# Optimization experiments

Measured on AMD Instinct MI355X. Metric: run time of the kernel, lower is better.

## Reference

```python
import jax, jax.numpy as jnp
import numpy as np

N_NODES = 100000
N_EDGES = 3200000
D = 128
B = 4


def gcn_conv(x, row, col, W, b, n):
    # PyG GCNConv: x' = D^{-1/2}(A+I)D^{-1/2} (x W) + b
    xw = x @ W  # [N, out]
    ones = jnp.ones((row.shape[0],), dtype=x.dtype)
    deg = jax.ops.segment_sum(ones, col, num_segments=n) + 1.0  # self-loop
    dinv = jax.lax.rsqrt(deg)  # deg > 0 because of self-loops
    norm = dinv[row] * dinv[col]  # [E]
    msg = xw[row] * norm[:, None]  # gather + scale
    agg = jax.ops.segment_sum(msg, col, num_segments=n)  # scatter-add
    agg = agg + (dinv * dinv)[:, None] * xw  # self-loop contribution
    return agg + b


def setup_inputs() -> dict:
    key = jax.random.key(0)
    ks = jax.random.split(key, 10)
    x = jax.random.normal(ks[0], (N_NODES, D), dtype=jnp.float32)
    edge_index = jax.random.randint(ks[1], (2, N_EDGES), 0, N_NODES, dtype=jnp.int64)
    question_embeddings = jax.random.normal(ks[2], (B, D), dtype=jnp.float32)
    s = 1.0 / np.sqrt(D)
    W1 = jax.random.uniform(ks[3], (D, D), jnp.float32, -s, s)
    b1 = jnp.zeros((D,), jnp.float32)
    W2 = jax.random.uniform(ks[4], (D, D), jnp.float32, -s, s)
    b2 = jnp.zeros((D,), jnp.float32)
    Wq = jax.random.uniform(ks[5], (D, D), jnp.float32, -s, s)
    bq = jax.random.uniform(ks[6], (D,), jnp.float32, -s, s)
    return {"x": x, "edge_index": edge_index, "question_embeddings": question_embeddings,
            "W1": W1, "b1": b1, "W2": W2, "b2": b2, "Wq": Wq, "bq": bq}


def reference(x, edge_index, question_embeddings, W1, b1, W2, b2, Wq, bq):
    n = x.shape[0]
    row, col = edge_index[0], edge_index[1]
    h = jax.nn.relu(gcn_conv(x, row, col, W1, b1, n))  # [N, H]
    h = gcn_conv(h, row, col, W2, b2, n)  # [N, H]
    q = question_embeddings @ Wq + bq  # [B, H]
    out = h[None, :, :] + q[:, None, :]  # [B, N, H]
    return jax.nn.log_softmax(out, axis=1)  # softmax over node dim (torch dim=1)
```

## Files before the change

### kernel.cpp

```cpp
#include <hip/hip_runtime.h>
#include <math.h>

#define DD 128
#define CT 4096
#define CAP 10240

typedef unsigned int uint;
typedef unsigned short u16;

typedef __attribute__((ext_vector_type(8))) __bf16 bf16x8;
typedef __attribute__((ext_vector_type(2))) __bf16 bf16x2;
typedef __attribute__((ext_vector_type(4))) float f32x4;
typedef __attribute__((ext_vector_type(4))) uint uint4v;
typedef __attribute__((ext_vector_type(8))) u16 u16x8;


__device__ inline uint bf16bits(float a) {
  uint u = __float_as_uint(a);
  return (u + 0x7fffu + ((u >> 16) & 1u)) >> 16;
}

__device__ inline uint pack_bf16x2(float a, float b) {
  bf16x2 t;
  t[0] = (__bf16)a;
  t[1] = (__bf16)b;
  return __builtin_bit_cast(uint, t);
}

__device__ inline float lo16f(uint u) { return __uint_as_float(u << 16); }
__device__ inline float hi16f(uint u) { return __uint_as_float(u & 0xffff0000u); }


__global__ __launch_bounds__(256) void k_coarse(const int* __restrict__ row,
                                                const int* __restrict__ col,
                                                int* __restrict__ gcursor,
                                                uint* __restrict__ coarse,
                                                int E, int NB) {
  __shared__ int hist[512];
  __shared__ int base[512];
  int tid = threadIdx.x;
  long e0 = (long)blockIdx.x * CT;
  int cnt = (int)min((long)CT, (long)E - e0);
  int cnt4 = cnt >> 2;
  const int4* c4p = (const int4*)(col + e0);
  const int4* r4p = (const int4*)(row + e0);
  for (int i = tid; i < NB; i += 256) hist[i] = 0;
  __syncthreads();
  for (int i = tid; i < cnt4; i += 256) {
    int4 c = c4p[i];
    atomicAdd(&hist[c.x >> 8], 1);
    atomicAdd(&hist[c.y >> 8], 1);
    atomicAdd(&hist[c.z >> 8], 1);
    atomicAdd(&hist[c.w >> 8], 1);
  }
  for (int i = (cnt4 << 2) + tid; i < cnt; i += 256) atomicAdd(&hist[col[e0 + i] >> 8], 1);
  __syncthreads();
  for (int i = tid; i < NB; i += 256) {
    base[i] = i * CAP + atomicAdd(&gcursor[i], hist[i]);
    hist[i] = 0;
  }
  __syncthreads();
  for (int i = tid; i < cnt4; i += 256) {
    int4 c = c4p[i];
    int4 r = r4p[i];
    int b;
    b = c.x >> 8; coarse[base[b] + atomicAdd(&hist[b], 1)] = ((uint)r.x << 8) | (uint)(c.x & 255);
    b = c.y >> 8; coarse[base[b] + atomicAdd(&hist[b], 1)] = ((uint)r.y << 8) | (uint)(c.y & 255);
    b = c.z >> 8; coarse[base[b] + atomicAdd(&hist[b], 1)] = ((uint)r.z << 8) | (uint)(c.z & 255);
    b = c.w >> 8; coarse[base[b] + atomicAdd(&hist[b], 1)] = ((uint)r.w << 8) | (uint)(c.w & 255);
  }
  for (int i = (cnt4 << 2) + tid; i < cnt; i += 256) {
    int c = col[e0 + i];
    int r = row[e0 + i];
    int b = c >> 8;
    coarse[base[b] + atomicAdd(&hist[b], 1)] = ((uint)r << 8) | (uint)(c & 255);
  }
}

__global__ __launch_bounds__(256) void k_finalize(const uint* __restrict__ coarse,
                                                  const int* __restrict__ gcursor,
                                                  int* __restrict__ offB,
                                                  int* __restrict__ offE,
                                                  float* __restrict__ dinv,
                                                  int* __restrict__ srt, int n) {
  __shared__ int hist[256];
  __shared__ int s[256];
  __shared__ int cur[256];
  int tid = threadIdx.x;
  int b = blockIdx.x;
  int base = b * CAP;
  int cnt = gcursor[b];
  int cnt4 = cnt >> 2;
  const uint4* e4p = (const uint4*)(coarse + base);
  int node0 = b << 8;
  hist[tid] = 0;
  __syncthreads();
  for (int i = tid; i < cnt4; i += 256) {
    uint4 e = e4p[i];
    atomicAdd(&hist[e.x & 255u], 1);
    atomicAdd(&hist[e.y & 255u], 1);
    atomicAdd(&hist[e.z & 255u], 1);
    atomicAdd(&hist[e.w & 255u], 1);
  }
  for (int i = (cnt4 << 2) + tid; i < cnt; i += 256) atomicAdd(&hist[coarse[base + i] & 255u], 1);
  __syncthreads();
  int deg = hist[tid];
  s[tid] = deg;
  __syncthreads();
  for (int o = 1; o < 256; o <<= 1) {
    int add = (tid >= o) ? s[tid - o] : 0;
    __syncthreads();
    s[tid] += add;
    __syncthreads();
  }
  int p0 = base + s[tid] - deg;
  int node = node0 + tid;
  if (node < n) {
    offB[node] = p0;
    offE[node] = p0 + deg;
    dinv[node] = rsqrtf(1.0f + (float)deg);
  }
  cur[tid] = p0;
  __syncthreads();
  for (int i = tid; i < cnt4; i += 256) {
    uint4 e = e4p[i];
    int pos;
    pos = atomicAdd(&cur[e.x & 255u], 1); srt[pos] = (int)(e.x & 0xFFFFFF00u);
    pos = atomicAdd(&cur[e.y & 255u], 1); srt[pos] = (int)(e.y & 0xFFFFFF00u);
    pos = atomicAdd(&cur[e.z & 255u], 1); srt[pos] = (int)(e.z & 0xFFFFFF00u);
    pos = atomicAdd(&cur[e.w & 255u], 1); srt[pos] = (int)(e.w & 0xFFFFFF00u);
  }
  for (int i = (cnt4 << 2) + tid; i < cnt; i += 256) {
    uint e = coarse[base + i];
    int pos = atomicAdd(&cur[e & 255u], 1);
    srt[pos] = (int)(e & 0xFFFFFF00u);
  }
}


__global__ __launch_bounds__(256) void k_prepw(const float* __restrict__ W1,
                                               const float* __restrict__ W2,
                                               u16* __restrict__ o1h, u16* __restrict__ o1l,
                                               u16* __restrict__ o2h, u16* __restrict__ o2l,
                                               int* __restrict__ gcursor, int NB) {
  if (blockIdx.x == 0)
    for (int i = threadIdx.x; i < NB; i += 256) gcursor[i] = 0;
  const float* W = blockIdx.x ? W2 : W1;
  u16* oh = blockIdx.x ? o2h : o1h;
  u16* ol = blockIdx.x ? o2l : o1l;
  for (int i = threadIdx.x; i < 16384; i += 256) {
    int k = i >> 7, c = i & 127;
    float v = W[i];
    uint hb = bf16bits(v);
    float hv = __uint_as_float(hb << 16);
    uint lb = bf16bits(v - hv);
    uint uidx = (((uint)c << 6) + ((uint)k >> 1)) ^ (((uint)c & 7u) << 2);
    int p = (int)((uidx << 1) | ((uint)k & 1u));
    oh[p] = (u16)hb;
    ol[p] = (u16)lb;
  }
}


template <int PRE>
__global__ __launch_bounds__(256, 2) void k_gemm(const float* __restrict__ X,
                                                 const uint* __restrict__ Xh,
                                                 const uint* __restrict__ Xl,
                                                 const u16* __restrict__ gWh,
                                                 const u16* __restrict__ gWl,
                                                 const float* __restrict__ dinv,
                                                 uint* __restrict__ msg, int n) {
  __shared__ uint Wh[8192];
  __shared__ uint Wl[8192];
  int tid = threadIdx.x;
  for (int i = tid; i < 2048; i += 256) ((uint4*)Wh)[i] = ((const uint4*)gWh)[i];
  for (int i = tid; i < 2048; i += 256) ((uint4*)Wl)[i] = ((const uint4*)gWl)[i];

  int lane = tid & 63, wv = tid >> 6;
  int s_ = lane & 15, g = lane >> 4;
  int row0 = blockIdx.x * 128 + wv * 32;

  f32x4 acc[2][8];
#pragma unroll
  for (int a = 0; a < 2; a++)
#pragma unroll
    for (int b = 0; b < 8; b++) acc[a][b] = (f32x4)0.f;

  __syncthreads();

#pragma unroll
  for (int kc = 0; kc < 4; kc++) {
    uint4v ah[2], al[2];
#pragma unroll
    for (int sub = 0; sub < 2; sub++) {
      int r = row0 + sub * 16 + s_;
      if (PRE) {
        uint4 hv = make_uint4(0u, 0u, 0u, 0u), lv = hv;
        if (r < n) {
          hv = ((const uint4*)Xh)[(size_t)r * 16 + kc * 4 + g];
          lv = ((const uint4*)Xl)[(size_t)r * 16 + kc * 4 + g];
        }
        ah[sub][0] = hv.x; ah[sub][1] = hv.y; ah[sub][2] = hv.z; ah[sub][3] = hv.w;
        al[sub][0] = lv.x; al[sub][1] = lv.y; al[sub][2] = lv.z; al[sub][3] = lv.w;
      } else {
        float4 v0, v1;
        if (r < n) {
          const float* xp = X + (size_t)r * DD + kc * 32 + g * 8;
          v0 = ((const float4*)xp)[0];
          v1 = ((const float4*)xp)[1];
        } else {
          v0 = make_float4(0.f, 0.f, 0.f, 0.f);
          v1 = v0;
        }
        uint p0 = pack_bf16x2(v0.x, v0.y), p1 = pack_bf16x2(v0.z, v0.w);
        uint p2 = pack_bf16x2(v1.x, v1.y), p3 = pack_bf16x2(v1.z, v1.w);
        ah[sub][0] = p0; ah[sub][1] = p1; ah[sub][2] = p2; ah[sub][3] = p3;
        al[sub][0] = pack_bf16x2(v0.x - lo16f(p0), v0.y - hi16f(p0));
        al[sub][1] = pack_bf16x2(v0.z - lo16f(p1), v0.w - hi16f(p1));
        al[sub][2] = pack_bf16x2(v1.x - lo16f(p2), v1.y - hi16f(p2));
        al[sub][3] = pack_bf16x2(v1.z - lo16f(p3), v1.w - hi16f(p3));
      }
    }
    int koff2 = (kc * 32 + g * 8) >> 1;
#pragma unroll
    for (int ct = 0; ct < 8; ct++) {
      int c = ct * 16 + s_;
      int uo = (int)(((uint)(c << 6) + (uint)koff2) ^ (((uint)c & 7u) << 2));
      bf16x8 bh = __builtin_bit_cast(bf16x8, *(const u16x8*)&Wh[uo]);
      bf16x8 bl = __builtin_bit_cast(bf16x8, *(const u16x8*)&Wl[uo]);
#pragma unroll
      for (int sub = 0; sub < 2; sub++) {
        bf16x8 av = __builtin_bit_cast(bf16x8, ah[sub]);
        bf16x8 lv = __builtin_bit_cast(bf16x8, al[sub]);
        acc[sub][ct] = __builtin_amdgcn_mfma_f32_16x16x32_bf16(av, bh, acc[sub][ct], 0, 0, 0);
        acc[sub][ct] = __builtin_amdgcn_mfma_f32_16x16x32_bf16(lv, bh, acc[sub][ct], 0, 0, 0);
        acc[sub][ct] = __builtin_amdgcn_mfma_f32_16x16x32_bf16(av, bl, acc[sub][ct], 0, 0, 0);
      }
    }
  }

#pragma unroll
  for (int sub = 0; sub < 2; sub++) {
#pragma unroll
    for (int q = 0; q < 4; q++) {
      int rq = row0 + sub * 16 + g * 4 + q;
      if (rq < n) {
        float di = dinv[rq];
        uint* mrow = msg + (size_t)rq * 64;
#pragma unroll
        for (int ct = 0; ct < 4; ct++) {
          uint u = pack_bf16x2(acc[sub][ct][q] * di, acc[sub][ct + 4][q] * di);
          mrow[ct * 16 + s_] = u;
        }
      }
    }
  }
}


__global__ __launch_bounds__(256) void k_agg(const uint* __restrict__ msg,
                                             const int* __restrict__ srt,
                                             const int* __restrict__ offB,
                                             const int* __restrict__ offE,
                                             const float* __restrict__ dinv,
                                             const float* __restrict__ bias,
                                             float* __restrict__ out,
                                             uint* __restrict__ hh,
                                             uint* __restrict__ hl, int n, int relu) {
  int lane = threadIdx.x & 63;
  int s_ = lane & 15, g = lane >> 4;
  int node = blockIdx.x * 4 + (threadIdx.x >> 6);
  if (node >= n) return;
  int beg = offB[node], end = offE[node];
  float a0 = 0.f, a1 = 0.f, a2 = 0.f, a3 = 0.f, a4 = 0.f, a5 = 0.f, a6 = 0.f, a7 = 0.f;
  const char* mb = (const char*)msg + s_ * 16;
  for (int t = beg; t < end; t += 64) {
    int nt = end - t;
    if (nt > 64) nt = 64;
    int boff = srt[t + (lane < nt ? lane : nt - 1)];
    for (int k = 0; k < nt; k += 32) {
      uint4 r[8];
      if (k + 32 <= nt) {
#pragma unroll
        for (int u = 0; u < 8; u++) {
          int bo = __shfl(boff, k + u * 4 + g);
          r[u] = *(const uint4*)(mb + (uint)bo);
        }
#pragma unroll
        for (int u = 0; u < 8; u++) {
          a0 += __uint_as_float(r[u].x << 16); a4 += __uint_as_float(r[u].x & 0xffff0000u);
          a1 += __uint_as_float(r[u].y << 16); a5 += __uint_as_float(r[u].y & 0xffff0000u);
          a2 += __uint_as_float(r[u].z << 16); a6 += __uint_as_float(r[u].z & 0xffff0000u);
          a3 += __uint_as_float(r[u].w << 16); a7 += __uint_as_float(r[u].w & 0xffff0000u);
        }
      } else {
#pragma unroll
        for (int u = 0; u < 8; u++) {
          int e = k + u * 4 + g;
          int bo = __shfl(boff, e < nt ? e : nt - 1);
          r[u] = *(const uint4*)(mb + (uint)bo);
          if (e >= nt) r[u] = make_uint4(0u, 0u, 0u, 0u);
        }
#pragma unroll
        for (int u = 0; u < 8; u++) {
          a0 += __uint_as_float(r[u].x << 16); a4 += __uint_as_float(r[u].x & 0xffff0000u);
          a1 += __uint_as_float(r[u].y << 16); a5 += __uint_as_float(r[u].y & 0xffff0000u);
          a2 += __uint_as_float(r[u].z << 16); a6 += __uint_as_float(r[u].z & 0xffff0000u);
          a3 += __uint_as_float(r[u].w << 16); a7 += __uint_as_float(r[u].w & 0xffff0000u);
        }
      }
    }
  }
#define RED(x) x += __shfl_xor(x, 16); x += __shfl_xor(x, 32);
  RED(a0) RED(a1) RED(a2) RED(a3) RED(a4) RED(a5) RED(a6) RED(a7)
#undef RED
  const uint4* m4 = (const uint4*)msg;
  uint4 rs = m4[(size_t)node * 16 + s_];
  a0 += __uint_as_float(rs.x << 16); a4 += __uint_as_float(rs.x & 0xffff0000u);
  a1 += __uint_as_float(rs.y << 16); a5 += __uint_as_float(rs.y & 0xffff0000u);
  a2 += __uint_as_float(rs.z << 16); a6 += __uint_as_float(rs.z & 0xffff0000u);
  a3 += __uint_as_float(rs.w << 16); a7 += __uint_as_float(rs.w & 0xffff0000u);
  float di = dinv[node];
  if (g < 2) {
    float4 bv = ((const float4*)(bias + (g ? 64 : 0)))[s_];
    float o0, o1, o2, o3;
    if (g == 0) {
      o0 = di * a0 + bv.x; o1 = di * a1 + bv.y; o2 = di * a2 + bv.z; o3 = di * a3 + bv.w;
    } else {
      o0 = di * a4 + bv.x; o1 = di * a5 + bv.y; o2 = di * a6 + bv.z; o3 = di * a7 + bv.w;
    }
    if (relu) {
      o0 = fmaxf(o0, 0.f); o1 = fmaxf(o1, 0.f); o2 = fmaxf(o2, 0.f); o3 = fmaxf(o3, 0.f);
      uint h0 = pack_bf16x2(o0, o1), h1 = pack_bf16x2(o2, o3);
      uint l0 = pack_bf16x2(o0 - lo16f(h0), o1 - hi16f(h0));
      uint l1 = pack_bf16x2(o2 - lo16f(h1), o3 - hi16f(h1));
      int mb2 = node * 64 + (g ? 32 : 0) + 2 * s_;
      *(uint2*)(hh + mb2) = make_uint2(h0, h1);
      *(uint2*)(hl + mb2) = make_uint2(l0, l1);
    } else {
      *(float4*)(out + (size_t)node * DD + (g ? 64 : 0) + 4 * s_) = make_float4(o0, o1, o2, o3);
    }
  }
}


__global__ __launch_bounds__(256) void k_colstat(const float* __restrict__ h, int n,
                                                 float* __restrict__ PM,
                                                 float* __restrict__ PS) {
  __shared__ float sm[128], ss[128];
  int d = threadIdx.x & 127, sub = threadIdx.x >> 7;
  float m = -3.4e38f, s = 0.f;
  for (int r = blockIdx.x * 2 + sub; r < n; r += gridDim.x * 2) {
    float v = h[(size_t)r * DD + d];
    float nm = fmaxf(m, v);
    s = s * __expf(m - nm) + __expf(v - nm);
    m = nm;
  }
  if (sub) { sm[d] = m; ss[d] = s; }
  __syncthreads();
  if (!sub) {
    float m2 = sm[d], s2 = ss[d];
    float nm = fmaxf(m, m2);
    float so = s * __expf(m - nm) + s2 * __expf(m2 - nm);
    PM[blockIdx.x * 128 + d] = nm;
    PS[blockIdx.x * 128 + d] = so;
  }
}

__global__ __launch_bounds__(64) void k_lsemerge(const float* __restrict__ PM,
                                                 const float* __restrict__ PS,
                                                 float* __restrict__ L, int nb) {
  int d = blockIdx.x;
  int lane = threadIdx.x;
  float m = -3.4e38f, s = 0.f;
  for (int p = lane; p < nb; p += 64) {
    float m2 = PM[p * 128 + d], s2 = PS[p * 128 + d];
    float nm = fmaxf(m, m2);
    s = s * __expf(m - nm) + s2 * __expf(m2 - nm);
    m = nm;
  }
#pragma unroll
  for (int o = 1; o < 64; o <<= 1) {
    float m2 = __shfl_xor(m, o), s2 = __shfl_xor(s, o);
    float nm = fmaxf(m, m2);
    s = s * __expf(m - nm) + s2 * __expf(m2 - nm);
    m = nm;
  }
  if (lane == 0) L[d] = m + logf(s);
}


__global__ __launch_bounds__(256) void k_final(const float* __restrict__ h,
                                               const float* __restrict__ L,
                                               float* __restrict__ out, int n, int B) {
  int idx = blockIdx.x * 256 + threadIdx.x;
  int nd4 = n * 32;
  if (idx >= nd4) return;
  int c4 = idx & 31;
  float4 hv = ((const float4*)h)[idx];
  float4 lv = ((const float4*)L)[c4];
  float4 r = make_float4(hv.x - lv.x, hv.y - lv.y, hv.z - lv.z, hv.w - lv.w);
  float4* o = (float4*)out;
  for (int b = 0; b < B; b++) o[(size_t)idx + (size_t)b * nd4] = r;
}


extern "C" void kernel_launch(void* const* d_in, const int* in_sizes, int n_in,
                              void* d_out, int out_size, void* d_ws, size_t ws_size,
                              hipStream_t stream) {
  const float* x  = (const float*)d_in[0];
  const int*   ei = (const int*)d_in[1];
  const float* W1 = (const float*)d_in[3];
  const float* b1 = (const float*)d_in[4];
  const float* W2 = (const float*)d_in[5];
  const float* b2 = (const float*)d_in[6];

  int n = in_sizes[0] / DD;
  int E = in_sizes[1] / 2;
  int B = out_size / (n * DD);
  const int* row = ei;
  const int* col = ei + E;

  float* out = (float*)d_out;
  size_t nd = (size_t)n * DD;
  int NB = (n + 255) / 256;
  size_t CAPN = (size_t)NB * CAP;
  uint* hh = (uint*)out;
  uint* hl = hh + (size_t)n * 64;
  float* bufB = out + nd;
  int* srt = (int*)(out + 2 * nd);
  uint* coarse = (uint*)(srt + CAPN);
  uint* msg = (uint*)coarse;
  char* sm = (char*)(out + 3 * nd);
  auto alloc = [&](size_t bytes) -> char* {
    char* p = sm;
    sm += (bytes + 63) & ~(size_t)63;
    return p;
  };
  float* dinv = (float*)alloc(sizeof(float) * n);
  int* offB = (int*)alloc(sizeof(int) * n);
  int* offE = (int*)alloc(sizeof(int) * n);
  int* gcursor = (int*)alloc(sizeof(int) * NB);
  u16* wt1h = (u16*)alloc(32768);
  u16* wt1l = (u16*)alloc(32768);
  u16* wt2h = (u16*)alloc(32768);
  u16* wt2l = (u16*)alloc(32768);
  float* PM = (float*)alloc(sizeof(float) * 512 * 128);
  float* PS = (float*)alloc(sizeof(float) * 512 * 128);
  float* L = (float*)d_ws;

  int gC = (E + CT - 1) / CT;

  k_prepw<<<2, 256, 0, stream>>>(W1, W2, wt1h, wt1l, wt2h, wt2l, gcursor, NB);
  k_coarse<<<gC, 256, 0, stream>>>(row, col, gcursor, coarse, E, NB);
  k_finalize<<<NB, 256, 0, stream>>>(coarse, gcursor, offB, offE, dinv, srt, n);

  int gG = (n + 127) / 128;
  k_gemm<0><<<gG, 256, 0, stream>>>(x, nullptr, nullptr, wt1h, wt1l, dinv, msg, n);
  k_agg<<<(n + 3) / 4, 256, 0, stream>>>(msg, srt, offB, offE, dinv, b1, bufB, hh, hl, n, 1);
  k_gemm<1><<<gG, 256, 0, stream>>>(nullptr, hh, hl, wt2h, wt2l, dinv, msg, n);
  k_agg<<<(n + 3) / 4, 256, 0, stream>>>(msg, srt, offB, offE, dinv, b2, bufB, hh, hl, n, 0);

  k_colstat<<<512, 256, 0, stream>>>(bufB, n, PM, PS);
  k_lsemerge<<<128, 64, 0, stream>>>(PM, PS, L, 512);
  k_final<<<(n * 32 + 255) / 256, 256, 0, stream>>>(bufB, L, out, n, B);
}
```

Baseline: 681.2 us.

## Quantize layer-1 messages to int8 with per-group exponent scales for gather

The first GEMM now writes its normalized output as int8 values, with a shared power-of-two exponent for each group of 8 features, instead of bf16. The first aggregation gathers 8-byte chunks plus a scale byte per edge and dequantizes on the fly. This halves the bytes moved in the random-access neighbor gather over 3.2M edges. The cost is precision: int8 with a block exponent is coarser than bf16. The hidden-state layout also changes from interleaved-pair to strided u16 stores.

```diff
diff --git a/kernel.cpp b/kernel.cpp
--- a/kernel.cpp
+++ b/kernel.cpp
@@ -7,6 +7,7 @@
 
 typedef unsigned int uint;
 typedef unsigned short u16;
+typedef unsigned char u8;
 
 typedef __attribute__((ext_vector_type(8))) __bf16 bf16x8;
 typedef __attribute__((ext_vector_type(2))) __bf16 bf16x2;
@@ -162,14 +163,16 @@
 }
 
 
-template <int PRE>
+template <int PRE, int OUT8>
 __global__ __launch_bounds__(256, 2) void k_gemm(const float* __restrict__ X,
-                                                 const uint* __restrict__ Xh,
-                                                 const uint* __restrict__ Xl,
+                                                 const u16* __restrict__ Xh,
+                                                 const u16* __restrict__ Xl,
                                                  const u16* __restrict__ gWh,
                                                  const u16* __restrict__ gWl,
                                                  const float* __restrict__ dinv,
-                                                 uint* __restrict__ msg, int n) {
+                                                 uint* __restrict__ msg,
+                                                 u8* __restrict__ msg8,
+                                                 u8* __restrict__ scl, int n) {
   __shared__ uint Wh[8192];
   __shared__ uint Wl[8192];
   int tid = threadIdx.x;
@@ -197,8 +200,8 @@
       if (PRE) {
         uint4 hv = make_uint4(0u, 0u, 0u, 0u), lv = hv;
         if (r < n) {
-          hv = ((const uint4*)Xh)[(size_t)r * 16 + kc * 4 + g];
-          lv = ((const uint4*)Xl)[(size_t)r * 16 + kc * 4 + g];
+          hv = *(const uint4*)(Xh + (size_t)r * 128 + kc * 32 + g * 8);
+          lv = *(const uint4*)(Xl + (size_t)r * 128 + kc * 32 + g * 8);
         }
         ah[sub][0] = hv.x; ah[sub][1] = hv.y; ah[sub][2] = hv.z; ah[sub][3] = hv.w;
         al[sub][0] = lv.x; al[sub][1] = lv.y; al[sub][2] = lv.z; al[sub][3] = lv.w;
@@ -246,11 +249,37 @@
       int rq = row0 + sub * 16 + g * 4 + q;
       if (rq < n) {
         float di = dinv[rq];
-        uint* mrow = msg + (size_t)rq * 64;
-#pragma unroll
-        for (int ct = 0; ct < 4; ct++) {
-          uint u = pack_bf16x2(acc[sub][ct][q] * di, acc[sub][ct + 4][q] * di);
-          mrow[ct * 16 + s_] = u;
+        if (OUT8) {
+          float v[8];
+#pragma unroll
+          for (int ct = 0; ct < 8; ct++) v[ct] = acc[sub][ct][q] * di;
+          float m = fmaxf(fmaxf(fmaxf(fabsf(v[0]), fabsf(v[1])), fmaxf(fabsf(v[2]), fabsf(v[3]))),
+                          fmaxf(fmaxf(fabsf(v[4]), fabsf(v[5])), fmaxf(fabsf(v[6]), fabsf(v[7]))));
+          m = fmaxf(m, 1e-30f);
+          uint ex = (__float_as_uint(m) >> 23) & 255u;
+          float sf = __uint_as_float((260u - ex) << 23);
+          uint b0 = 0u, b1 = 0u;
+#pragma unroll
+          for (int j = 0; j < 4; j++) {
+            int qi = (int)rintf(v[j] * sf);
+            qi = qi > 127 ? 127 : (qi < -127 ? -127 : qi);
+            b0 |= ((uint)qi & 255u) << (8 * j);
+          }
+#pragma unroll
+          for (int j = 0; j < 4; j++) {
+            int qi = (int)rintf(v[4 + j] * sf);
+            qi = qi > 127 ? 127 : (qi < -127 ? -127 : qi);
+            b1 |= ((uint)qi & 255u) << (8 * j);
+          }
+          *(uint2*)(msg8 + (size_t)rq * 128 + s_ * 8) = make_uint2(b0, b1);
+          scl[(size_t)rq * 16 + s_] = (u8)ex;
+        } else {
+          uint* mrow = msg + (size_t)rq * 64;
+#pragma unroll
+          for (int ct = 0; ct < 4; ct++) {
+            uint u = pack_bf16x2(acc[sub][ct][q] * di, acc[sub][ct + 4][q] * di);
+            mrow[ct * 16 + s_] = u;
+          }
         }
       }
     }
@@ -258,15 +287,18 @@
 }
 
 
+template <int IN8>
 __global__ __launch_bounds__(256) void k_agg(const uint* __restrict__ msg,
+                                             const u8* __restrict__ msg8,
+                                             const u8* __restrict__ scl,
                                              const int* __restrict__ srt,
                                              const int* __restrict__ offB,
                                              const int* __restrict__ offE,
                                              const float* __restrict__ dinv,
                                              const float* __restrict__ bias,
                                              float* __restrict__ out,
-                                             uint* __restrict__ hh,
-                                             uint* __restrict__ hl, int n, int relu) {
+                                             u16* __restrict__ hh,
+                                             u16* __restrict__ hl, int n) {
   int lane = threadIdx.x & 63;
   int s_ = lane & 15, g = lane >> 4;
   int node = blockIdx.x * 4 + (threadIdx.x >> 6);
@@ -274,17 +306,53 @@
   int beg = offB[node], end = offE[node];
   float a0 = 0.f, a1 = 0.f, a2 = 0.f, a3 = 0.f, a4 = 0.f, a5 = 0.f, a6 = 0.f, a7 = 0.f;
   const char* mb = (const char*)msg + s_ * 16;
+  const u8* m8 = msg8 + s_ * 8;
+  const u8* sb = scl + s_;
   for (int t = beg; t < end; t += 64) {
     int nt = end - t;
     if (nt > 64) nt = 64;
     int boff = srt[t + (lane < nt ? lane : nt - 1)];
     for (int k = 0; k < nt; k += 32) {
-      uint4 r[8];
-      if (k + 32 <= nt) {
+      if (IN8) {
+        uint2 r[8];
+        float fs[8];
 #pragma unroll
         for (int u = 0; u < 8; u++) {
-          int bo = __shfl(boff, k + u * 4 + g);
-          r[u] = *(const uint4*)(mb + (uint)bo);
+          int e = k + u * 4 + g;
+          int bo = __shfl(boff, e < nt ? e : nt - 1);
+          r[u] = *(const uint2*)(m8 + ((uint)bo >> 1));
+          fs[u] = __uint_as_float(((uint)sb[(uint)bo >> 4] - 6u) << 23);
+          if (e >= nt) { r[u].x = 0u; r[u].y = 0u; }
+        }
+#pragma unroll
+        for (int u = 0; u < 8; u++) {
+          float f = fs[u];
+          uint x = r[u].x, y = r[u].y;
+          a0 += (float)((int)(x << 24) >> 24) * f;
+          a1 += (float)((int)(x << 16) >> 24) * f;
+          a2 += (float)((int)(x << 8) >> 24) * f;
+          a3 += (float)((int)x >> 24) * f;
+          a4 += (float)((int)(y << 24) >> 24) * f;
+          a5 += (float)((int)(y << 16) >> 24) * f;
+          a6 += (float)((int)(y << 8) >> 24) * f;
+          a7 += (float)((int)y >> 24) * f;
+        }
+      } else {
+        uint4 r[8];
+        if (k + 32 <= nt) {
+#pragma unroll
+          for (int u = 0; u < 8; u++) {
+            int bo = __shfl(boff, k + u * 4 + g);
+            r[u] = *(const uint4*)(mb + (uint)bo);
+          }
+        } else {
+#pragma unroll
+          for (int u = 0; u < 8; u++) {
+            int e = k + u * 4 + g;
+            int bo = __shfl(boff, e < nt ? e : nt - 1);
+            r[u] = *(const uint4*)(mb + (uint)bo);
+            if (e >= nt) r[u] = make_uint4(0u, 0u, 0u, 0u);
+          }
         }
 #pragma unroll
         for (int u = 0; u < 8; u++) {
@@ -293,51 +361,55 @@
           a2 += __uint_as_float(r[u].z << 16); a6 += __uint_as_float(r[u].z & 0xffff0000u);
           a3 += __uint_as_float(r[u].w << 16); a7 += __uint_as_float(r[u].w & 0xffff0000u);
         }
-      } else {
-#pragma unroll
-        for (int u = 0; u < 8; u++) {
-          int e = k + u * 4 + g;
-          int bo = __shfl(boff, e < nt ? e : nt - 1);
-          r[u] = *(const uint4*)(mb + (uint)bo);
-          if (e >= nt) r[u] = make_uint4(0u, 0u, 0u, 0u);
-        }
-#pragma unroll
-        for (int u = 0; u < 8; u++) {
-          a0 += __uint_as_float(r[u].x << 16); a4 += __uint_as_float(r[u].x & 0xffff0000u);
-          a1 += __uint_as_float(r[u].y << 16); a5 += __uint_as_float(r[u].y & 0xffff0000u);
-          a2 += __uint_as_float(r[u].z << 16); a6 += __uint_as_float(r[u].z & 0xffff0000u);
-          a3 += __uint_as_float(r[u].w << 16); a7 += __uint_as_float(r[u].w & 0xffff0000u);
-        }
       }
     }
   }
 #define RED(x) x += __shfl_xor(x, 16); x += __shfl_xor(x, 32);
   RED(a0) RED(a1) RED(a2) RED(a3) RED(a4) RED(a5) RED(a6) RED(a7)
 #undef RED
-  const uint4* m4 = (const uint4*)msg;
-  uint4 rs = m4[(size_t)node * 16 + s_];
-  a0 += __uint_as_float(rs.x << 16); a4 += __uint_as_float(rs.x & 0xffff0000u);
-  a1 += __uint_as_float(rs.y << 16); a5 += __uint_as_float(rs.y & 0xffff0000u);
-  a2 += __uint_as_float(rs.z << 16); a6 += __uint_as_float(rs.z & 0xffff0000u);
-  a3 += __uint_as_float(rs.w << 16); a7 += __uint_as_float(rs.w & 0xffff0000u);
   float di = dinv[node];
-  if (g < 2) {
-    float4 bv = ((const float4*)(bias + (g ? 64 : 0)))[s_];
-    float o0, o1, o2, o3;
-    if (g == 0) {
-      o0 = di * a0 + bv.x; o1 = di * a1 + bv.y; o2 = di * a2 + bv.z; o3 = di * a3 + bv.w;
-    } else {
-      o0 = di * a4 + bv.x; o1 = di * a5 + bv.y; o2 = di * a6 + bv.z; o3 = di * a7 + bv.w;
+  if (IN8) {
+    uint bo = (uint)node << 8;
+    uint2 rs = *(const uint2*)(m8 + (bo >> 1));
+    float f = __uint_as_float(((uint)sb[bo >> 4] - 6u) << 23);
+    a0 += (float)((int)(rs.x << 24) >> 24) * f;
+    a1 += (float)((int)(rs.x << 16) >> 24) * f;
+    a2 += (float)((int)(rs.x << 8) >> 24) * f;
+    a3 += (float)((int)rs.x >> 24) * f;
+    a4 += (float)((int)(rs.y << 24) >> 24) * f;
+    a5 += (float)((int)(rs.y << 16) >> 24) * f;
+    a6 += (float)((int)(rs.y << 8) >> 24) * f;
+    a7 += (float)((int)rs.y >> 24) * f;
+    if (g < 2) {
+      float o0 = g ? a4 : a0, o1 = g ? a5 : a1, o2 = g ? a6 : a2, o3 = g ? a7 : a3;
+      int dbase = g * 64 + s_;
+      o0 = fmaxf(di * o0 + bias[dbase], 0.f);
+      o1 = fmaxf(di * o1 + bias[dbase + 16], 0.f);
+      o2 = fmaxf(di * o2 + bias[dbase + 32], 0.f);
+      o3 = fmaxf(di * o3 + bias[dbase + 48], 0.f);
+      size_t rb = (size_t)node * 128 + dbase;
+      uint h0 = bf16bits(o0), h1 = bf16bits(o1), h2 = bf16bits(o2), h3 = bf16bits(o3);
+      hh[rb] = (u16)h0; hh[rb + 16] = (u16)h1; hh[rb + 32] = (u16)h2; hh[rb + 48] = (u16)h3;
+      hl[rb] = (u16)bf16bits(o0 - __uint_as_float(h0 << 16));
+      hl[rb + 16] = (u16)bf16bits(o1 - __uint_as_float(h1 << 16));
+      hl[rb + 32] = (u16)bf16bits(o2 - __uint_as_float(h2 << 16));
+      hl[rb + 48] = (u16)bf16bits(o3 - __uint_as_float(h3 << 16));
     }
-    if (relu) {
-      o0 = fmaxf(o0, 0.f); o1 = fmaxf(o1, 0.f); o2 = fmaxf(o2, 0.f); o3 = fmaxf(o3, 0.f);
-      uint h0 = pack_bf16x2(o0, o1), h1 = pack_bf16x2(o2, o3);
-      uint l0 = pack_bf16x2(o0 - lo16f(h0), o1 - hi16f(h0));
-      uint l1 = pack_bf16x2(o2 - lo16f(h1), o3 - hi16f(h1));
-      int mb2 = node * 64 + (g ? 32 : 0) + 2 * s_;
-      *(uint2*)(hh + mb2) = make_uint2(h0, h1);
-      *(uint2*)(hl + mb2) = make_uint2(l0, l1);
-    } else {
+  } else {
+    const uint4* m4 = (const uint4*)msg;
+    uint4 rs = m4[(size_t)node * 16 + s_];
+    a0 += __uint_as_float(rs.x << 16); a4 += __uint_as_float(rs.x & 0xffff0000u);
+    a1 += __uint_as_float(rs.y << 16); a5 += __uint_as_float(rs.y & 0xffff0000u);
+    a2 += __uint_as_float(rs.z << 16); a6 += __uint_as_float(rs.z & 0xffff0000u);
+    a3 += __uint_as_float(rs.w << 16); a7 += __uint_as_float(rs.w & 0xffff0000u);
+    if (g < 2) {
+      float4 bv = ((const float4*)(bias + (g ? 64 : 0)))[s_];
+      float o0, o1, o2, o3;
+      if (g == 0) {
+        o0 = di * a0 + bv.x; o1 = di * a1 + bv.y; o2 = di * a2 + bv.z; o3 = di * a3 + bv.w;
+      } else {
+        o0 = di * a4 + bv.x; o1 = di * a5 + bv.y; o2 = di * a6 + bv.z; o3 = di * a7 + bv.w;
+      }
       *(float4*)(out + (size_t)node * DD + (g ? 64 : 0) + 4 * s_) = make_float4(o0, o1, o2, o3);
     }
   }
@@ -425,11 +497,13 @@
   size_t nd = (size_t)n * DD;
   int NB = (n + 255) / 256;
   size_t CAPN = (size_t)NB * CAP;
-  uint* hh = (uint*)out;
-  uint* hl = hh + (size_t)n * 64;
+  u16* hh = (u16*)out;
+  u16* hl = hh + (size_t)n * 128;
   float* bufB = out + nd;
   int* srt = (int*)(out + 2 * nd);
   uint* coarse = (uint*)(srt + CAPN);
+  u8* msg8 = (u8*)coarse;
+  u8* scl = msg8 + (size_t)n * 128;
   uint* msg = (uint*)coarse;
   char* sm = (char*)(out + 3 * nd);
   auto alloc = [&](size_t bytes) -> char* {
@@ -456,10 +530,15 @@
   k_finalize<<<NB, 256, 0, stream>>>(coarse, gcursor, offB, offE, dinv, srt, n);
 
   int gG = (n + 127) / 128;
-  k_gemm<0><<<gG, 256, 0, stream>>>(x, nullptr, nullptr, wt1h, wt1l, dinv, msg, n);
-  k_agg<<<(n + 3) / 4, 256, 0, stream>>>(msg, srt, offB, offE, dinv, b1, bufB, hh, hl, n, 1);
-  k_gemm<1><<<gG, 256, 0, stream>>>(nullptr, hh, hl, wt2h, wt2l, dinv, msg, n);
-  k_agg<<<(n + 3) / 4, 256, 0, stream>>>(msg, srt, offB, offE, dinv, b2, bufB, hh, hl, n, 0);
+  int gA = (n + 3) / 4;
+  k_gemm<0, 1><<<gG, 256, 0, stream>>>(x, nullptr, nullptr, wt1h, wt1l, dinv,
+                                       nullptr, msg8, scl, n);
+  k_agg<1><<<gA, 256, 0, stream>>>(nullptr, msg8, scl, srt, offB, offE, dinv, b1,
+                                   nullptr, hh, hl, n);
+  k_gemm<1, 0><<<gG, 256, 0, stream>>>(nullptr, hh, hl, wt2h, wt2l, dinv,
+                                       msg, nullptr, nullptr, n);
+  k_agg<0><<<gA, 256, 0, stream>>>(msg, nullptr, nullptr, srt, offB, offE, dinv, b2,
+                                   bufB, nullptr, nullptr, n);
 
   k_colstat<<<512, 256, 0, stream>>>(bufB, n, PM, PS);
   k_lsemerge<<<128, 64, 0, stream>>>(PM, PS, L, 512);
```

Measured after the change: 652.3 us. -4.2%, faster.
